# Performance work log

Hardware: AMD Instinct MI355X
Metric: run time of the kernel (lower is better)

The kernel has to match this reference:

```python
import jax, jax.numpy as jnp
import numpy as np

D = 128          # kg_emb_dim
H = 8            # mha_n_heads
N = 20000        # sub-graph nodes per modality
NNZ = 500000     # incidence entries per modality
E = 5000         # hyperedges per modality
C = 50           # context entities
NENT = 50000     # n_entity (rec vocab)


def hyperconv(x, theta, bias, nodes, edges, num_edges):
    # PyG-style HypergraphConv: out = D^-1 H B^-1 H^T (X Theta) + b
    xt = x @ theta                                             # [N, D]
    ones = jnp.ones(nodes.shape[0], xt.dtype)
    e_sum = jax.ops.segment_sum(xt[nodes], edges, num_segments=num_edges)   # [E, D]
    e_deg = jax.ops.segment_sum(ones, edges, num_segments=num_edges)        # [E]
    m = e_sum / jnp.maximum(e_deg, 1.0)[:, None]               # hyperedge means
    n_sum = jax.ops.segment_sum(m[edges], nodes, num_segments=x.shape[0])   # [N, D]
    n_deg = jax.ops.segment_sum(ones, nodes, num_segments=x.shape[0])       # [N]
    return n_sum / jnp.maximum(n_deg, 1.0)[:, None] + bias


def mha(q_x, kv_x, Wq, bq, Wk, bk, Wv, bv, Wo, bo):
    # torch.nn.MultiheadAttention math, batch of 1 (squeezed)
    dh = D // H
    q = (q_x @ Wq + bq).reshape(-1, H, dh)
    k = (kv_x @ Wk + bk).reshape(-1, H, dh)
    v = (kv_x @ Wv + bv).reshape(-1, H, dh)
    scores = jnp.einsum('qhd,khd->hqk', q, k) / jnp.sqrt(jnp.asarray(dh, q.dtype))
    attn = jax.nn.softmax(scores, axis=-1)
    out = jnp.einsum('hqk,khd->qhd', attn, v).reshape(-1, D)
    return out @ Wo + bo


def self_attn(h, a, b):
    # SelfAttentionBatch: softmax(tanh(h a) b) weighted sum over rows
    e = (jnp.tanh(h @ a) @ b)[:, 0]
    return jax.nn.softmax(e) @ h


def setup_inputs() -> dict:
    ks = jax.random.split(jax.random.key(0), 32)
    s = D ** (-0.5)
    inp = {
        'item_emb':   jax.random.normal(ks[0], (N, D), jnp.float32) * s,
        'entity_emb': jax.random.normal(ks[1], (N, D), jnp.float32) * s,
        'word_emb':   jax.random.normal(ks[2], (N, D), jnp.float32) * s,
        'context_entity': jax.random.normal(ks[3], (C, D), jnp.float32) * s,
        'theta_item':   jax.random.normal(ks[4], (D, D), jnp.float32) * s,
        'bias_item':    jax.random.normal(ks[5], (D,), jnp.float32) * 0.02,
        'theta_entity': jax.random.normal(ks[6], (D, D), jnp.float32) * s,
        'bias_entity':  jax.random.normal(ks[7], (D,), jnp.float32) * 0.02,
        'theta_word':   jax.random.normal(ks[8], (D, D), jnp.float32) * s,
        'bias_word':    jax.random.normal(ks[9], (D,), jnp.float32) * 0.02,
        'Wq': jax.random.normal(ks[10], (D, D), jnp.float32) * s,
        'bq': jax.random.normal(ks[11], (D,), jnp.float32) * 0.02,
        'Wk': jax.random.normal(ks[12], (D, D), jnp.float32) * s,
        'bk': jax.random.normal(ks[13], (D,), jnp.float32) * 0.02,
        'Wv': jax.random.normal(ks[14], (D, D), jnp.float32) * s,
        'bv': jax.random.normal(ks[15], (D,), jnp.float32) * 0.02,
        'Wo': jax.random.normal(ks[16], (D, D), jnp.float32) * s,
        'bo': jax.random.normal(ks[17], (D,), jnp.float32) * 0.02,
        'a_his': jax.random.normal(ks[18], (D, D), jnp.float32) * s,
        'b_his': jax.random.normal(ks[19], (D, 1), jnp.float32) * s,
        'a_kg':  jax.random.normal(ks[20], (D, D), jnp.float32) * s,
        'b_kg':  jax.random.normal(ks[21], (D, 1), jnp.float32) * s,
        'rec_W': jax.random.normal(ks[22], (D, NENT), jnp.float32) * s,
        'rec_b': jax.random.normal(ks[23], (NENT,), jnp.float32) * 0.02,
        'item_nodes':   jax.random.randint(ks[24], (NNZ,), 0, N, jnp.int32),
        'item_edges':   jax.random.randint(ks[25], (NNZ,), 0, E, jnp.int32),
        'entity_nodes': jax.random.randint(ks[26], (NNZ,), 0, N, jnp.int32),
        'entity_edges': jax.random.randint(ks[27], (NNZ,), 0, E, jnp.int32),
        'word_nodes':   jax.random.randint(ks[28], (NNZ,), 0, N, jnp.int32),
        'word_edges':   jax.random.randint(ks[29], (NNZ,), 0, E, jnp.int32),
    }
    return inp


def reference(item_emb, entity_emb, word_emb, context_entity,
              theta_item, bias_item, theta_entity, bias_entity, theta_word, bias_word,
              Wq, bq, Wk, bk, Wv, bv, Wo, bo,
              a_his, b_his, a_kg, b_kg, rec_W, rec_b,
              item_nodes, item_edges, entity_nodes, entity_edges, word_nodes, word_edges):
    ih = hyperconv(item_emb, theta_item, bias_item, item_nodes, item_edges, E)
    eh = hyperconv(entity_emb, theta_entity, bias_entity, entity_nodes, entity_edges, E)
    wh = hyperconv(word_emb, theta_word, bias_word, word_nodes, word_edges, E)
    related = jnp.concatenate([ih, eh, wh], axis=0)            # [3N, D]
    # MHItemAttention: context queries attend over related embeddings
    attentive = mha(context_entity, related, Wq, bq, Wk, bk, Wv, bv, Wo, bo)  # [C, D]
    u = self_attn(attentive, a_his, b_his)                     # [D]
    user = jnp.concatenate([context_entity, u[None]], axis=0)  # [C+1, D]
    user_repr = self_attn(user, a_kg, b_kg)                    # [D]
    scores = user_repr @ rec_W + rec_b                         # [NENT]
    return scores
```

## Files before the change

kernel.cpp:

```cpp
#include <hip/hip_runtime.h>
#include <hip/hip_bf16.h>

#define D_ 128
#define H_ 8
#define N_ 20000
#define NNZ_ 500000
#define E_ 5000
#define C_ 50
#define NENT_ 50000
#define NK_ (3*N_)
#define CAPE_ 192
#define CAPN_ 64
#define ENT_PB 4096
#define NBKT 157
#define BCAP 3648
#define ABLK 123
#define NCH3 118
#define KVBLK 235
#define BINA_B (3*ABLK)
#define NBB (3*NBKT)
#define EGB 3752

struct Ptr3f { const float* p[3]; };
struct Ptr3i { const int* p[3]; };
struct GemmB { const float* A[3]; const float* W[3]; unsigned short* C[3]; };

typedef short bf16x8 __attribute__((ext_vector_type(8)));
typedef float f32x4  __attribute__((ext_vector_type(4)));
typedef float f32x2  __attribute__((ext_vector_type(2)));

__device__ __forceinline__ unsigned short f2b(float f){
  unsigned u = __float_as_uint(f);
  u += 0x7FFFu + ((u>>16)&1u);
  return (unsigned short)(u>>16);
}
__device__ __forceinline__ unsigned pk2(float a, float b){
  return (unsigned)f2b(a) | ((unsigned)f2b(b) << 16);
}
__device__ __forceinline__ float blo(unsigned u){ return __uint_as_float(u<<16); }
__device__ __forceinline__ float bhi(unsigned u){ return __uint_as_float(u & 0xFFFF0000u); }

#define GBATCH(SRCB, SREG, LBASE) { \
  uint4 uu[8]; \
  _Pragma("unroll") \
  for (int kk=0;kk<8;kk++){ \
    int off = __shfl(SREG, (LBASE) + 4*kk + rgrp); \
    uu[kk] = *(const uint4*)((SRCB) + off); \
  } \
  _Pragma("unroll") \
  for (int kk=0;kk<8;kk++){ \
    a01 += (f32x2){blo(uu[kk].x), bhi(uu[kk].x)}; \
    a23 += (f32x2){blo(uu[kk].y), bhi(uu[kk].y)}; \
    a45 += (f32x2){blo(uu[kk].z), bhi(uu[kk].z)}; \
    a67 += (f32x2){blo(uu[kk].w), bhi(uu[kk].w)}; \
  } }

#define PB_PACK 7500
#define PB_Z    7628
#define PB_Q    7629
#define PB_CTX  7693
#define PB_TOT  7743
__global__ __launch_bounds__(256) void prep_binA(Ptr3f xs, unsigned short* __restrict__ xb,
    const float* __restrict__ Wk, const float* __restrict__ Wv, unsigned short* __restrict__ bfB,
    unsigned short* __restrict__ mzero,
    const float* __restrict__ ctx, const float* __restrict__ Wq, const float* __restrict__ bq,
    unsigned short* __restrict__ bfQ,
    const float* __restrict__ a2, const float* __restrict__ b2, float* __restrict__ e2,
    Ptr3i nodes, Ptr3i edges,
    unsigned* __restrict__ pe_part, unsigned* __restrict__ pn_part,
    int* __restrict__ gcnt_e, int* __restrict__ gcnt_n)
{
  const int t = threadIdx.x;
  if (blockIdx.x < BINA_B){
    __shared__ unsigned lbin[ENT_PB];
    __shared__ int cnt[256], off[256];
    __shared__ int gbase[NBKT];
    __shared__ int wsum[4];
    const int mod = blockIdx.x / ABLK;
    const int xblk = blockIdx.x - mod*ABLK;
    const int* nd = nodes.p[mod];
    const int* ed = edges.p[mod];
    const int base = xblk * ENT_PB;
    const int lane = t & 63, w = t >> 6;

    int myn[16], mye[16], pos[16];
    #pragma unroll
    for (int k=0;k<16;k++){
      int i = base + t + k*256;
      if (i < NNZ_){ myn[k]=nd[i]; mye[k]=ed[i]; }
      else { myn[k]=-1; mye[k]=-1; }
    }

    cnt[t] = 0;
    __syncthreads();
    #pragma unroll
    for (int k=0;k<16;k++)
      if (mye[k] >= 0) pos[k] = atomicAdd(&cnt[mye[k]>>5], 1);
    __syncthreads();
    {
      int v = cnt[t], s = v;
      #pragma unroll
      for (int d=1; d<64; d<<=1){ int u=__shfl_up(s,d); if (lane>=d) s+=u; }
      if (lane==63) wsum[w]=s;
      __syncthreads();
      int wb=0;
      for (int i=0;i<w;i++) wb+=wsum[i];
      off[t] = wb + s - v;
      __syncthreads();
    }
    #pragma unroll
    for (int k=0;k<16;k++)
      if (mye[k] >= 0)
        lbin[off[mye[k]>>5] + pos[k]] = ((unsigned)mye[k] << 15) | (unsigned)myn[k];
    if (t < NBKT && cnt[t] > 0) gbase[t] = atomicAdd(&gcnt_e[mod*NBKT + t], cnt[t]);
    __syncthreads();
    {
      int total = off[255];
      unsigned* dstreg = pe_part + (size_t)mod*NBKT*BCAP;
      for (int i=t; i<total; i+=256){
        unsigned pk = lbin[i];
        int b = pk >> 20;
        int gp = gbase[b] + (i - off[b]);
        if (gp < BCAP) dstreg[(size_t)b*BCAP + gp] = pk;
      }
    }
    __syncthreads();

    cnt[t] = 0;
    __syncthreads();
    #pragma unroll
    for (int k=0;k<16;k++)
      if (myn[k] >= 0) pos[k] = atomicAdd(&cnt[myn[k]>>7], 1);
    __syncthreads();
    {
      int v = cnt[t], s = v;
      #pragma unroll
      for (int d=1; d<64; d<<=1){ int u=__shfl_up(s,d); if (lane>=d) s+=u; }
      if (lane==63) wsum[w]=s;
      __syncthreads();
      int wb=0;
      for (int i=0;i<w;i++) wb+=wsum[i];
      off[t] = wb + s - v;
      __syncthreads();
    }
    #pragma unroll
    for (int k=0;k<16;k++)
      if (myn[k] >= 0)
        lbin[off[myn[k]>>7] + pos[k]] = ((unsigned)myn[k] << 13) | (unsigned)mye[k];
    if (t < NBKT && cnt[t] > 0) gbase[t] = atomicAdd(&gcnt_n[mod*NBKT + t], cnt[t]);
    __syncthreads();
    {
      int total = off[255];
      unsigned* dstreg = pn_part + (size_t)mod*NBKT*BCAP;
      for (int i=t; i<total; i+=256){
        unsigned pk = lbin[i];
        int b = pk >> 20;
        int gp = gbase[b] + (i - off[b]);
        if (gp < BCAP) dstreg[(size_t)b*BCAP + gp] = pk;
      }
    }
    return;
  }

  int bid = blockIdx.x - BINA_B;
  if (bid < PB_PACK){
    int mod = bid / 2500, blk = bid - mod*2500;
    int i4 = blk*256 + t;
    float4 v = *(const float4*)(xs.p[mod] + (size_t)i4*4);
    ushort4 o; o.x=f2b(v.x); o.y=f2b(v.y); o.z=f2b(v.z); o.w=f2b(v.w);
    *(ushort4*)(xb + (size_t)mod*N_*D_ + (size_t)i4*4) = o;
  } else if (bid < PB_Z){
    int idx = (bid - PB_PACK)*256 + t;
    int j  = idx & 7;
    int L  = (idx >> 3) & 63;
    int kb = (idx >> 9) & 3;
    int tt = idx >> 11;
    int k = kb*32 + (L>>4)*8 + j;
    int x = L & 15;
    float v = (tt < 8) ? Wk[(size_t)k*128 + tt*16 + x] : Wv[(size_t)k*128 + (tt-8)*16 + x];
    bfB[idx] = f2b(v);
  } else if (bid == PB_Z){
    if (t < 64)       ((unsigned*)(xb    + (size_t)60000*128))[t]    = 0u;
    else if (t < 128) ((unsigned*)(mzero + (size_t)15000*128))[t-64] = 0u;
  } else if (bid < PB_CTX){
    int idx = (bid - PB_Q)*256 + t;
    int j  = idx & 7;
    int L  = (idx >> 3) & 63;
    int qt = (idx >> 9) & 3;
    int h  = idx >> 11;
    int k  = ((L>>4)&3)*8 + j;
    int q  = qt*16 + (L & 15);
    float val = 0.f;
    if (k < 16 && q < C_){
      const float* cr = ctx + (size_t)q*128;
      const float* wc = Wq + h*16 + k;
      float s0=0.f,s1=0.f,s2=0.f,s3=0.f;
      for (int d=0; d<128; d+=4){
        s0 = fmaf(cr[d],   wc[(size_t) d   *128], s0);
        s1 = fmaf(cr[d+1], wc[(size_t)(d+1)*128], s1);
        s2 = fmaf(cr[d+2], wc[(size_t)(d+2)*128], s2);
        s3 = fmaf(cr[d+3], wc[(size_t)(d+3)*128], s3);
      }
      val = 0.25f * (s0+s1+s2+s3 + bq[h*16+k]);
    }
    bfQ[idx] = f2b(val);
  } else {
    __shared__ float row[128];
    __shared__ float ps[128][2];
    __shared__ float red[2];
    int q = bid - PB_CTX;
    if (t < 128) row[t] = ctx[(size_t)q*128 + t];
    __syncthreads();
    int c = t & 127, half = t >> 7;
    float s = 0.f;
    int d0 = half*64;
    for (int d=d0; d<d0+64; d+=4){
      s = fmaf(row[d],   a2[(size_t) d   *128 + c], s);
      s = fmaf(row[d+1], a2[(size_t)(d+1)*128 + c], s);
      s = fmaf(row[d+2], a2[(size_t)(d+2)*128 + c], s);
      s = fmaf(row[d+3], a2[(size_t)(d+3)*128 + c], s);
    }
    ps[c][half] = s;
    __syncthreads();
    if (t < 128){
      float v = tanhf(ps[t][0] + ps[t][1]) * b2[t];
      #pragma unroll
      for (int k=32; k>=1; k>>=1) v += __shfl_xor(v, k);
      if ((t & 63) == 0) red[t>>6] = v;
    }
    __syncthreads();
    if (t == 0) e2[q] = red[0] + red[1];
  }
}

__global__ __launch_bounds__(256) void binB_e(const unsigned* __restrict__ pe_part,
    const int* __restrict__ gcnt_e, int* __restrict__ cnt_all,
    unsigned short* __restrict__ e_slot)
{
  __shared__ unsigned short ls[32*CAPE_];
  __shared__ int lc[32];
  const int mod = blockIdx.y, b = blockIdx.x, t = threadIdx.x;
  {
    unsigned short dmy = (unsigned short)(60000 - mod*20000);
    unsigned dd = (unsigned)dmy * 0x10001u;
    unsigned* lsu32 = (unsigned*)ls;
    for (int i=t; i<32*CAPE_/2; i+=256) lsu32[i] = dd;
  }
  if (t < 32) lc[t] = 0;
  __syncthreads();
  int cnt = gcnt_e[mod*NBKT + b];
  if (cnt > BCAP) cnt = BCAP;
  const unsigned* src = pe_part + ((size_t)mod*NBKT + b)*BCAP;
  for (int i=t; i<cnt; i+=256){
    unsigned pk = src[i];
    int el = (pk >> 15) - b*32;
    int n  = pk & 0x7FFF;
    int p = atomicAdd(&lc[el], 1);
    if (p < CAPE_) ls[el*CAPE_ + p] = (unsigned short)n;
  }
  __syncthreads();
  int rows = E_ - b*32; if (rows > 32) rows = 32;
  if (t < rows) cnt_all[mod*(E_+N_) + b*32 + t] = lc[t];
  const unsigned* lsu = (const unsigned*)ls;
  unsigned* dst = (unsigned*)(e_slot + ((size_t)mod*E_ + b*32)*CAPE_);
  int tot = rows*CAPE_/2;
  for (int i=t; i<tot; i+=256) dst[i] = lsu[i];
}

__global__ __launch_bounds__(256) void egather_binbn(const unsigned short* __restrict__ xb,
    const int* __restrict__ cnt_all, const unsigned short* __restrict__ e_slot,
    float* __restrict__ m_mean,
    const unsigned* __restrict__ pn_part, const int* __restrict__ gcnt_n,
    int* __restrict__ cnt_all_w, unsigned short* __restrict__ n_slot)
{
  __shared__ unsigned short ls[128*CAPN_];
  __shared__ int lc[128];
  const int t = threadIdx.x;
  if (blockIdx.x < NBB){
    const int mod = blockIdx.x / NBKT, b = blockIdx.x - mod*NBKT;
    {
      unsigned short dmy = (unsigned short)(15000 - mod*5000);
      unsigned dd = (unsigned)dmy * 0x10001u;
      unsigned* lsu32 = (unsigned*)ls;
      for (int i=t; i<128*CAPN_/2; i+=256) lsu32[i] = dd;
    }
    if (t < 128) lc[t] = 0;
    __syncthreads();
    int cnt = gcnt_n[mod*NBKT + b];
    if (cnt > BCAP) cnt = BCAP;
    const unsigned* src = pn_part + ((size_t)mod*NBKT + b)*BCAP;
    for (int i=t; i<cnt; i+=256){
      unsigned pk = src[i];
      int nl = (pk >> 13) - b*128;
      int e  = pk & 0x1FFF;
      int p = atomicAdd(&lc[nl], 1);
      if (p < CAPN_) ls[nl*CAPN_ + p] = (unsigned short)e;
    }
    __syncthreads();
    int rows = N_ - b*128; if (rows > 128) rows = 128;
    if (t < rows) cnt_all_w[mod*(E_+N_) + E_ + b*128 + t] = lc[t];
    const unsigned* lsu = (const unsigned*)ls;
    unsigned* dst = (unsigned*)(n_slot + ((size_t)mod*N_ + b*128)*CAPN_);
    int tot = rows*CAPN_/2;
    for (int i=t; i<tot; i+=256) dst[i] = lsu[i];
    return;
  }

  const int bb = blockIdx.x - NBB;
  const int x = bb & 7, k = bb >> 3;
  int mod, r;
  if (x < 6){
    mod = x / 3;
    int li = x - mod*3;
    int c = 417 - (li == 2);
    if (k < c){
      r = k*3 + li;
    } else {
      int hg = 52*x + (x >= 3) + (k - c);
      mod = 2; r = 938 + hg;
      if (r >= E_/4) return;
    }
  } else {
    mod = 2; r = k*2 + (x - 6);
  }
  const int w = t >> 6, lane = t & 63;
  const int rgrp = lane >> 4, dl = lane & 15;
  const int e = r*4 + w;
  const char* xt8 = (const char*)(xb + (size_t)mod*N_*D_) + dl*8*2;
  int cnt = cnt_all[mod*(E_+N_) + e];
  int c2 = (cnt < CAPE_) ? cnt : CAPE_;
  int c2p = (c2 + 31) & ~31;
  const unsigned short* slot = e_slot + ((size_t)mod*E_ + e)*CAPE_;
  int sv0 = ((int)slot[lane]) << 8;
  int sv1 = ((int)slot[64 + lane]) << 8;
  int sv2 = ((int)slot[128 + lane]) << 8;
  f32x2 a01={0.f,0.f}, a23={0.f,0.f}, a45={0.f,0.f}, a67={0.f,0.f};

  if (c2p > 0)   GBATCH(xt8, sv0, 0);
  if (c2p > 32)  GBATCH(xt8, sv0, 32);
  if (c2p > 64)  GBATCH(xt8, sv1, 0);
  if (c2p > 96)  GBATCH(xt8, sv1, 32);
  if (c2p > 128) GBATCH(xt8, sv2, 0);
  if (c2p > 160) GBATCH(xt8, sv2, 32);

  float a0=a01.x, a1=a01.y, a2=a23.x, a3=a23.y, a4=a45.x, a5=a45.y, a6=a67.x, a7=a67.y;
  #pragma unroll
  for (int s=16; s<=32; s<<=1){
    a0 += __shfl_xor(a0, s); a1 += __shfl_xor(a1, s);
    a2 += __shfl_xor(a2, s); a3 += __shfl_xor(a3, s);
    a4 += __shfl_xor(a4, s); a5 += __shfl_xor(a5, s);
    a6 += __shfl_xor(a6, s); a7 += __shfl_xor(a7, s);
  }
  if (rgrp == 0){
    float inv = 1.f / fmaxf((float)cnt, 1.f);
    float* dst = m_mean + ((size_t)mod*E_ + e)*128 + dl*8;
    float4 o1; o1.x=a0*inv; o1.y=a1*inv; o1.z=a2*inv; o1.w=a3*inv;
    float4 o2; o2.x=a4*inv; o2.y=a5*inv; o2.z=a6*inv; o2.w=a7*inv;
    *(float4*)dst = o1;
    *(float4*)(dst + 4) = o2;
  }
}

__global__ __launch_bounds__(256) void gemm_b(GemmB g, int M)
{
  const float* A = g.A[blockIdx.y];
  const float* W = g.W[blockIdx.y];
  unsigned short* Cout = g.C[blockIdx.y];
  __shared__ float As[64][33];
  __shared__ float Ws[32][128];
  const int t  = threadIdx.x;
  const int br = blockIdx.x * 64;
  const int r0 = (t >> 5) * 8;
  const int c0 = (t & 31) * 4;
  const int lr = t >> 2;
  const int lk = (t & 3) * 8;
  const int wk = t >> 5;

  float acc[8][4];
  #pragma unroll
  for (int i=0;i<8;i++){ acc[i][0]=0.f; acc[i][1]=0.f; acc[i][2]=0.f; acc[i][3]=0.f; }

  for (int kb=0; kb<128; kb+=32){
    float av[8];
    const int grow = br + lr;
    if (grow < M){
      const float* p = A + (size_t)grow*128 + kb + lk;
      float4 a = ((const float4*)p)[0], b = ((const float4*)p)[1];
      av[0]=a.x;av[1]=a.y;av[2]=a.z;av[3]=a.w;av[4]=b.x;av[5]=b.y;av[6]=b.z;av[7]=b.w;
    } else {
      #pragma unroll
      for (int j=0;j<8;j++) av[j]=0.f;
    }
    float4 wv4[4];
    #pragma unroll
    for (int kk=0;kk<4;kk++) wv4[kk] = *(const float4*)&W[(size_t)(kb + wk + kk*8)*128 + c0];

    __syncthreads();
    #pragma unroll
    for (int j=0;j<8;j++) As[lr][lk+j] = av[j];
    #pragma unroll
    for (int kk=0;kk<4;kk++) *(float4*)&Ws[wk + kk*8][c0] = wv4[kk];
    __syncthreads();

    #pragma unroll
    for (int k=0;k<32;k++){
      float4 wv = *(const float4*)&Ws[k][c0];
      #pragma unroll
      for (int i=0;i<8;i++){
        float a = As[r0+i][k];
        acc[i][0] = fmaf(a, wv.x, acc[i][0]);
        acc[i][1] = fmaf(a, wv.y, acc[i][1]);
        acc[i][2] = fmaf(a, wv.z, acc[i][2]);
        acc[i][3] = fmaf(a, wv.w, acc[i][3]);
      }
    }
  }

  #pragma unroll
  for (int i=0;i<8;i++){
    int gr = br + r0 + i;
    if (gr < M){
      ushort4 o;
      o.x=f2b(acc[i][0]); o.y=f2b(acc[i][1]); o.z=f2b(acc[i][2]); o.w=f2b(acc[i][3]);
      *(ushort4*)(Cout + (size_t)gr*128 + c0) = o;
    }
  }
}

__global__ __launch_bounds__(256) void n_gather_g(const unsigned short* __restrict__ m_buf,
    const int* __restrict__ cnt_all, const unsigned short* __restrict__ n_slot,
    Ptr3f biases, unsigned short* __restrict__ relbf)
{
  const int mod = blockIdx.y;
  const int t = threadIdx.x, w = t >> 6, lane = t & 63;
  const int g = lane >> 4, dl = lane & 15;
  const int n = blockIdx.x*16 + w*4 + g;
  const char* mb = (const char*)(m_buf + (size_t)mod*E_*D_) + dl*16;
  int cnt = cnt_all[mod*(E_+N_) + E_ + n];
  int c2 = (cnt < CAPN_) ? cnt : CAPN_;
  int m = c2;
  m = max(m, __shfl_xor(m, 16));
  m = max(m, __shfl_xor(m, 32));
  int m8 = (m + 7) & ~7;
  const unsigned short* slot = n_slot + ((size_t)mod*N_ + n)*CAPN_;
  f32x2 a01={0.f,0.f}, a23={0.f,0.f}, a45={0.f,0.f}, a67={0.f,0.f};

  for (int j=0; j<m8; j+=8){
    uint4 sv = *(const uint4*)(slot + j);
    int o0 = (int)(sv.x & 0xFFFFu) << 8, o1 = (int)(sv.x >> 16) << 8;
    int o2 = (int)(sv.y & 0xFFFFu) << 8, o3 = (int)(sv.y >> 16) << 8;
    int o4 = (int)(sv.z & 0xFFFFu) << 8, o5 = (int)(sv.z >> 16) << 8;
    int o6 = (int)(sv.w & 0xFFFFu) << 8, o7 = (int)(sv.w >> 16) << 8;
    uint4 u0 = *(const uint4*)(mb + o0);
    uint4 u1 = *(const uint4*)(mb + o1);
    uint4 u2 = *(const uint4*)(mb + o2);
    uint4 u3 = *(const uint4*)(mb + o3);
    uint4 u4 = *(const uint4*)(mb + o4);
    uint4 u5 = *(const uint4*)(mb + o5);
    uint4 u6 = *(const uint4*)(mb + o6);
    uint4 u7 = *(const uint4*)(mb + o7);
    a01 += (f32x2){blo(u0.x), bhi(u0.x)}; a23 += (f32x2){blo(u0.y), bhi(u0.y)};
    a45 += (f32x2){blo(u0.z), bhi(u0.z)}; a67 += (f32x2){blo(u0.w), bhi(u0.w)};
    a01 += (f32x2){blo(u1.x), bhi(u1.x)}; a23 += (f32x2){blo(u1.y), bhi(u1.y)};
    a45 += (f32x2){blo(u1.z), bhi(u1.z)}; a67 += (f32x2){blo(u1.w), bhi(u1.w)};
    a01 += (f32x2){blo(u2.x), bhi(u2.x)}; a23 += (f32x2){blo(u2.y), bhi(u2.y)};
    a45 += (f32x2){blo(u2.z), bhi(u2.z)}; a67 += (f32x2){blo(u2.w), bhi(u2.w)};
    a01 += (f32x2){blo(u3.x), bhi(u3.x)}; a23 += (f32x2){blo(u3.y), bhi(u3.y)};
    a45 += (f32x2){blo(u3.z), bhi(u3.z)}; a67 += (f32x2){blo(u3.w), bhi(u3.w)};
    a01 += (f32x2){blo(u4.x), bhi(u4.x)}; a23 += (f32x2){blo(u4.y), bhi(u4.y)};
    a45 += (f32x2){blo(u4.z), bhi(u4.z)}; a67 += (f32x2){blo(u4.w), bhi(u4.w)};
    a01 += (f32x2){blo(u5.x), bhi(u5.x)}; a23 += (f32x2){blo(u5.y), bhi(u5.y)};
    a45 += (f32x2){blo(u5.z), bhi(u5.z)}; a67 += (f32x2){blo(u5.w), bhi(u5.w)};
    a01 += (f32x2){blo(u6.x), bhi(u6.x)}; a23 += (f32x2){blo(u6.y), bhi(u6.y)};
    a45 += (f32x2){blo(u6.z), bhi(u6.z)}; a67 += (f32x2){blo(u6.w), bhi(u6.w)};
    a01 += (f32x2){blo(u7.x), bhi(u7.x)}; a23 += (f32x2){blo(u7.y), bhi(u7.y)};
    a45 += (f32x2){blo(u7.z), bhi(u7.z)}; a67 += (f32x2){blo(u7.w), bhi(u7.w)};
  }

  float inv = 1.f / fmaxf((float)cnt, 1.f);
  const float* bs = biases.p[mod] + dl*8;
  uint4 o;
  o.x = pk2(a01.x*inv + bs[0], a01.y*inv + bs[1]);
  o.y = pk2(a23.x*inv + bs[2], a23.y*inv + bs[3]);
  o.z = pk2(a45.x*inv + bs[4], a45.y*inv + bs[5]);
  o.w = pk2(a67.x*inv + bs[6], a67.y*inv + bs[7]);
  *(uint4*)(relbf + ((size_t)mod*N_ + n)*128 + dl*8) = o;
}

__global__ __launch_bounds__(256) void gemm_kv_mfma(const unsigned short* __restrict__ relbf,
    const unsigned short* __restrict__ bfB, const float* __restrict__ bk,
    const float* __restrict__ bv, unsigned short* __restrict__ Kb,
    unsigned short* __restrict__ Vtg)
{
  __shared__ unsigned short Vs[128][72];
  const int t = threadIdx.x, w = t >> 6, L = t & 63;
  const int m = L & 15, quad = L >> 4, x = m;
  const int rowbase = blockIdx.x*256;

  for (int g = 0; g < 4; g++){
    const int j0 = rowbase + g*64 + w*16;

    bf16x8 a[4];
    {
      int row = j0 + m;
      int rowc = (row < NK_) ? row : (NK_-1);
      #pragma unroll
      for (int kb=0; kb<4; kb++)
        a[kb] = *(const bf16x8*)(relbf + (size_t)rowc*128 + kb*32 + quad*8);
    }

    f32x4 acc[16];
    #pragma unroll
    for (int tt=0; tt<16; tt++) acc[tt] = (f32x4){0.f,0.f,0.f,0.f};

    #pragma unroll
    for (int kb=0; kb<4; kb++){
      #pragma unroll
      for (int tt=0; tt<16; tt++){
        bf16x8 b = *(const bf16x8*)(bfB + (((tt*4 + kb)*64 + L) << 3));
        acc[tt] = __builtin_amdgcn_mfma_f32_16x16x32_bf16(a[kb], b, acc[tt], 0, 0, 0);
      }
    }

    #pragma unroll
    for (int tt=0; tt<8; tt++){
      float bias = bk[tt*16 + x];
      unsigned p0, p1;
      asm("v_cvt_pk_bf16_f32 %0, %1, %2" : "=v"(p0) : "v"(acc[tt][0]+bias), "v"(acc[tt][1]+bias));
      asm("v_cvt_pk_bf16_f32 %0, %1, %2" : "=v"(p1) : "v"(acc[tt][2]+bias), "v"(acc[tt][3]+bias));
      int jrb = j0 + quad*4;
      if (jrb + 3 < NK_){
        Kb[(((size_t)tt*NK_ + jrb    ) << 4) + x] = (unsigned short)p0;
        Kb[(((size_t)tt*NK_ + jrb + 1) << 4) + x] = (unsigned short)(p0 >> 16);
        Kb[(((size_t)tt*NK_ + jrb + 2) << 4) + x] = (unsigned short)p1;
        Kb[(((size_t)tt*NK_ + jrb + 3) << 4) + x] = (unsigned short)(p1 >> 16);
      } else {
        if (jrb     < NK_) Kb[(((size_t)tt*NK_ + jrb    ) << 4) + x] = (unsigned short)p0;
        if (jrb + 1 < NK_) Kb[(((size_t)tt*NK_ + jrb + 1) << 4) + x] = (unsigned short)(p0 >> 16);
        if (jrb + 2 < NK_) Kb[(((size_t)tt*NK_ + jrb + 2) << 4) + x] = (unsigned short)p1;
        if (jrb + 3 < NK_) Kb[(((size_t)tt*NK_ + jrb + 3) << 4) + x] = (unsigned short)(p1 >> 16);
      }
    }

    #pragma unroll
    for (int tt=8; tt<16; tt++){
      int h = tt - 8;
      float bias = bv[h*16 + x];
      unsigned p0, p1;
      asm("v_cvt_pk_bf16_f32 %0, %1, %2" : "=v"(p0) : "v"(acc[tt][0]+bias), "v"(acc[tt][1]+bias));
      asm("v_cvt_pk_bf16_f32 %0, %1, %2" : "=v"(p1) : "v"(acc[tt][2]+bias), "v"(acc[tt][3]+bias));
      int col = w*16 + quad*4;
      *(unsigned*)&Vs[h*16 + x][col]     = p0;
      *(unsigned*)&Vs[h*16 + x][col + 2] = p1;
    }
    __syncthreads();

    {
      int row = t >> 1, half = t & 1;
      int c0 = half*32;
      int jr0 = rowbase + g*64 + c0;
      const unsigned short* src = &Vs[row][c0];
      unsigned short* dstp = Vtg + (size_t)row*NK_ + jr0;
      if (jr0 + 31 < NK_){
        ((uint4*)dstp)[0] = ((const uint4*)src)[0];
        ((uint4*)dstp)[1] = ((const uint4*)src)[1];
        ((uint4*)dstp)[2] = ((const uint4*)src)[2];
        ((uint4*)dstp)[3] = ((const uint4*)src)[3];
      } else {
        for (int c=0; c<32; c++) if (jr0 + c < NK_) dstp[c] = src[c];
      }
    }
    __syncthreads();
  }
}

__global__ __launch_bounds__(256) void flash3(const unsigned short* __restrict__ Kb,
    const unsigned short* __restrict__ Vtg, const unsigned short* __restrict__ bfQ,
    float* __restrict__ part)
{
  __shared__ unsigned short P_lds[4][64][40];
  __shared__ float mbuf[4][64][18];
  const int c = blockIdx.x, h = blockIdx.y;
  const int t = threadIdx.x, w = t >> 6, L = t & 63;
  const int n = L & 15, quad = L >> 4;

  bf16x8 qb[4];
  #pragma unroll
  for (int qt=0; qt<4; qt++)
    qb[qt] = *(const bf16x8*)(bfQ + (((h*4 + qt)*64 + L) << 3));

  float Mc[4], Lc[4];
  f32x4 accq[4];
  #pragma unroll
  for (int qt=0; qt<4; qt++){ Mc[qt] = -INFINITY; Lc[qt] = 0.f; accq[qt] = (f32x4){0.f,0.f,0.f,0.f}; }

  const int base = c*512 + w*128;
  unsigned* Pw = (unsigned*)&P_lds[w][0][0];

  for (int tile=0; tile<4; tile++){
    const int j0 = base + tile*32;
    const bool dead = (j0 >= NK_);

    bf16x8 a0 = (bf16x8){0,0,0,0,0,0,0,0};
    bf16x8 a1 = a0;
    if (quad < 2){
      int k0 = j0 + n;      if (k0 > NK_-1) k0 = NK_-1;
      int k1 = j0 + 16 + n; if (k1 > NK_-1) k1 = NK_-1;
      a0 = *(const bf16x8*)(Kb + (((size_t)h*NK_ + k0) << 4) + quad*8);
      a1 = *(const bf16x8*)(Kb + (((size_t)h*NK_ + k1) << 4) + quad*8);
    }
    f32x4 s0[4], s1[4];
    #pragma unroll
    for (int qt=0; qt<4; qt++){
      s0[qt] = __builtin_amdgcn_mfma_f32_16x16x32_bf16(a0, qb[qt], (f32x4){0.f,0.f,0.f,0.f}, 0,0,0);
      s1[qt] = __builtin_amdgcn_mfma_f32_16x16x32_bf16(a1, qb[qt], (f32x4){0.f,0.f,0.f,0.f}, 0,0,0);
    }

    #pragma unroll
    for (int qt=0; qt<4; qt++){
      float mt = s0[qt][0];
      mt = fmaxf(mt, s0[qt][1]); mt = fmaxf(mt, s0[qt][2]); mt = fmaxf(mt, s0[qt][3]);
      mt = fmaxf(mt, s1[qt][0]); mt = fmaxf(mt, s1[qt][1]);
      mt = fmaxf(mt, s1[qt][2]); mt = fmaxf(mt, s1[qt][3]);
      mt = fmaxf(mt, __shfl_xor(mt, 16));
      mt = fmaxf(mt, __shfl_xor(mt, 32));
      float Mn = fmaxf(Mc[qt], mt);
      float corr = __expf(Mc[qt] - Mn);
      Mc[qt] = Mn;
      float p0[4], p1[4];
      #pragma unroll
      for (int r=0;r<4;r++){
        p0[r] = __expf(s0[qt][r] - Mn);
        p1[r] = __expf(s1[qt][r] - Mn);
      }
      if (dead){
        #pragma unroll
        for (int r=0;r<4;r++){ p0[r]=0.f; p1[r]=0.f; }
      }
      float lt = p0[0]+p0[1]+p0[2]+p0[3]+p1[0]+p1[1]+p1[2]+p1[3];
      lt += __shfl_xor(lt, 16);
      lt += __shfl_xor(lt, 32);
      Lc[qt] = Lc[qt]*corr + lt;
      int rb = (qt*16 + n)*20;
      Pw[rb + quad*2]     = pk2(p0[0], p0[1]);
      Pw[rb + quad*2 + 1] = pk2(p0[2], p0[3]);
      Pw[rb + 8 + quad*2]     = pk2(p1[0], p1[1]);
      Pw[rb + 8 + quad*2 + 1] = pk2(p1[2], p1[3]);
      #pragma unroll
      for (int r=0;r<4;r++){
        float cr = __shfl(corr, quad*4 + r);
        accq[qt][r] *= cr;
      }
    }
    __syncthreads();

    bf16x8 bv_;
    {
      int va = j0 + quad*8; if (va > NK_-8) va = NK_-8;
      bv_ = *(const bf16x8*)(Vtg + ((size_t)(h*16 + n))*NK_ + va);
    }
    #pragma unroll
    for (int qt=0; qt<4; qt++){
      bf16x8 pa = *(const bf16x8*)&P_lds[w][qt*16 + n][quad*8];
      accq[qt] = __builtin_amdgcn_mfma_f32_16x16x32_bf16(pa, bv_, accq[qt], 0,0,0);
    }
    __syncthreads();
  }

  #pragma unroll
  for (int qt=0; qt<4; qt++){
    #pragma unroll
    for (int r=0; r<4; r++)
      mbuf[w][qt*16 + quad*4 + r][2 + n] = accq[qt][r];
    if (quad == 0){
      mbuf[w][qt*16 + n][0] = Mc[qt];
      mbuf[w][qt*16 + n][1] = Lc[qt];
    }
  }
  __syncthreads();
  if (t < C_){
    float M = mbuf[0][t][0], Lm = mbuf[0][t][1];
    float A[16];
    #pragma unroll
    for (int i=0;i<16;i++) A[i] = mbuf[0][t][2+i];
    #pragma unroll
    for (int ww=1; ww<4; ww++){
      float pm = mbuf[ww][t][0], pl = mbuf[ww][t][1];
      if (pl > 0.f){
        float mn = fmaxf(M, pm);
        float c1 = __expf(M - mn), c2 = __expf(pm - mn);
        Lm = Lm*c1 + pl*c2;
        #pragma unroll
        for (int i=0;i<16;i++) A[i] = A[i]*c1 + mbuf[ww][t][2+i]*c2;
        M = mn;
      }
    }
    float* pp = part + ((size_t)(h*NCH3 + c)*C_ + t)*18;
    pp[0] = M; pp[1] = Lm;
    #pragma unroll
    for (int i=0;i<16;i++) pp[2+i] = A[i];
  }
}

__global__ __launch_bounds__(512) void merge_oproj_e1(const float* __restrict__ part,
    const float* __restrict__ Wo, const float* __restrict__ bo,
    const float* __restrict__ a1, const float* __restrict__ b1,
    float* __restrict__ attentive, float* __restrict__ e1)
{
  __shared__ float row[128];
  __shared__ float ps[128][4];
  __shared__ float orow[128];
  __shared__ float red[2];
  const int q = blockIdx.x, t = threadIdx.x;
  const int h = t >> 6, lane = t & 63;

  {
    float M = -1e30f, L = 0.f;
    float A[16];
    #pragma unroll
    for (int i=0;i<16;i++) A[i] = 0.f;

    #pragma unroll
    for (int cc=0; cc<2; cc++){
      int c = lane + cc*64;
      if (c < NCH3){
        const float* p = part + ((size_t)(h*NCH3 + c)*C_ + q)*18;
        float pm = p[0], pl = p[1];
        if (pl > 0.f){
          float Mn = fmaxf(M, pm);
          float w1 = __expf(M - Mn), w2 = __expf(pm - Mn);
          L = L*w1 + pl*w2;
          #pragma unroll
          for (int i=0;i<16;i++) A[i] = fmaf(A[i], w1, p[2+i]*w2);
          M = Mn;
        }
      }
    }
    #pragma unroll
    for (int d=32; d>=1; d>>=1){
      float pm = __shfl_xor(M, d);
      float pl = __shfl_xor(L, d);
      float Ao[16];
      #pragma unroll
      for (int i=0;i<16;i++) Ao[i] = __shfl_xor(A[i], d);
      float Mn = fmaxf(M, pm);
      float w1 = __expf(M - Mn), w2 = __expf(pm - Mn);
      L = L*w1 + pl*w2;
      #pragma unroll
      for (int i=0;i<16;i++) A[i] = fmaf(A[i], w1, Ao[i]*w2);
      M = Mn;
    }
    if (lane == 0){
      float invL = 1.f / L;
      #pragma unroll
      for (int i=0;i<16;i++) row[h*16 + i] = A[i]*invL;
    }
  }
  __syncthreads();

  const int c = t & 127, seg = t >> 7;
  {
    float s = 0.f;
    int d0 = seg*32;
    for (int d=d0; d<d0+32; d+=4){
      s = fmaf(row[d],   Wo[(size_t) d   *128 + c], s);
      s = fmaf(row[d+1], Wo[(size_t)(d+1)*128 + c], s);
      s = fmaf(row[d+2], Wo[(size_t)(d+2)*128 + c], s);
      s = fmaf(row[d+3], Wo[(size_t)(d+3)*128 + c], s);
    }
    ps[c][seg] = s;
  }
  __syncthreads();
  if (t < 128){
    float o = ps[t][0]+ps[t][1]+ps[t][2]+ps[t][3] + bo[t];
    attentive[(size_t)q*128 + t] = o;
    orow[t] = o;
  }
  __syncthreads();
  {
    float s = 0.f;
    int d0 = seg*32;
    for (int d=d0; d<d0+32; d+=4){
      s = fmaf(orow[d],   a1[(size_t) d   *128 + c], s);
      s = fmaf(orow[d+1], a1[(size_t)(d+1)*128 + c], s);
      s = fmaf(orow[d+2], a1[(size_t)(d+2)*128 + c], s);
      s = fmaf(orow[d+3], a1[(size_t)(d+3)*128 + c], s);
    }
    ps[c][seg] = s;
  }
  __syncthreads();
  if (t < 128){
    float v = tanhf(ps[t][0]+ps[t][1]+ps[t][2]+ps[t][3]) * b1[t];
    #pragma unroll
    for (int k=32; k>=1; k>>=1) v += __shfl_xor(v, k);
    if ((t & 63) == 0) red[t>>6] = v;
  }
  __syncthreads();
  if (t == 0) e1[q] = red[0] + red[1];
}

__global__ __launch_bounds__(256) void tail_scores(const float* __restrict__ attentive,
    const float* __restrict__ ctx, const float* __restrict__ a2, const float* __restrict__ b2,
    const float* __restrict__ e1, const float* __restrict__ e2,
    const float* __restrict__ recW, const float* __restrict__ recb, float* __restrict__ out)
{
  __shared__ float p[64];
  __shared__ float u[128];
  __shared__ float red[2];
  __shared__ float p2[64];
  __shared__ float ur[128];
  const int t = threadIdx.x;

  if (t == 0){
    float mx=-INFINITY;
    for (int i=0;i<C_;i++) mx=fmaxf(mx,e1[i]);
    float ss=0.f;
    for (int i=0;i<C_;i++){ p[i]=__expf(e1[i]-mx); ss+=p[i]; }
    float inv=1.f/ss;
    for (int i=0;i<C_;i++) p[i]*=inv;
  }
  __syncthreads();
  if (t < 128){
    float s=0.f;
    for (int r=0;r<C_;r++) s = fmaf(p[r], attentive[(size_t)r*128 + t], s);
    u[t] = s;
  }
  __syncthreads();
  if (t < 128){
    float s0=0.f,s1=0.f,s2=0.f,s3=0.f;
    for (int d=0; d<128; d+=4){
      s0 = fmaf(u[d],   a2[(size_t) d   *128 + t], s0);
      s1 = fmaf(u[d+1], a2[(size_t)(d+1)*128 + t], s1);
      s2 = fmaf(u[d+2], a2[(size_t)(d+2)*128 + t], s2);
      s3 = fmaf(u[d+3], a2[(size_t)(d+3)*128 + t], s3);
    }
    float v = tanhf(s0+s1+s2+s3) * b2[t];
    #pragma unroll
    for (int k=32; k>=1; k>>=1) v += __shfl_xor(v, k);
    if ((t & 63) == 0) red[t>>6] = v;
  }
  __syncthreads();
  if (t == 0){
    float elast = red[0] + red[1];
    float mx=elast;
    for (int i=0;i<C_;i++) mx=fmaxf(mx,e2[i]);
    float ss=0.f;
    for (int i=0;i<C_;i++){ p2[i]=__expf(e2[i]-mx); ss+=p2[i]; }
    float pl = __expf(elast-mx); ss += pl;
    float inv=1.f/ss;
    for (int i=0;i<C_;i++) p2[i]*=inv;
    p2[C_] = pl*inv;
  }
  __syncthreads();
  if (t < 128){
    float s=0.f;
    for (int r=0;r<C_;r++) s = fmaf(p2[r], ctx[(size_t)r*128 + t], s);
    s = fmaf(p2[C_], u[t], s);
    ur[t] = s;
  }
  __syncthreads();
  int j = blockIdx.x*256 + t;
  if (j < NENT_){
    float s0=0.f,s1=0.f,s2=0.f,s3=0.f;
    for (int d=0; d<128; d+=4){
      s0 = fmaf(ur[d],   recW[(size_t) d   *NENT_ + j], s0);
      s1 = fmaf(ur[d+1], recW[(size_t)(d+1)*NENT_ + j], s1);
      s2 = fmaf(ur[d+2], recW[(size_t)(d+2)*NENT_ + j], s2);
      s3 = fmaf(ur[d+3], recW[(size_t)(d+3)*NENT_ + j], s3);
    }
    out[j] = s0+s1+s2+s3 + recb[j];
  }
}

extern "C" void kernel_launch(void* const* d_in, const int* in_sizes, int n_in,
                              void* d_out, int out_size, void* d_ws, size_t ws_size,
                              hipStream_t stream)
{
  auto f32 = [&](int i){ return (const float*)d_in[i]; };
  Ptr3i nodes = {{(const int*)d_in[24], (const int*)d_in[26], (const int*)d_in[28]}};
  Ptr3i edges = {{(const int*)d_in[25], (const int*)d_in[27], (const int*)d_in[29]}};

  char* base = (char*)d_ws;
  int*   cnt_all = (int*)base;
  int*   gcnt_e  = (int*)(base + 300064);
  int*   gcnt_n  = gcnt_e + NBKT*3;
  unsigned short* n_slot = (unsigned short*)(base + 300064 + 4096);
  float* m_mean  = (float*)((char*)n_slot + 7680000);
  unsigned short* m_buf = (unsigned short*)((char*)m_mean + 7680000);
  unsigned short* relbf = (unsigned short*)((char*)m_buf + 3840256);
  unsigned short* bfB   = (unsigned short*)((char*)relbf + 15360000);
  unsigned short* bfQ   = (unsigned short*)((char*)bfB + 65536);
  float* attentive = (float*)((char*)bfQ + 32768);
  float* user_repr = (float*)((char*)attentive + 25600);
  float* e1buf     = user_repr + 128;
  float* e2buf     = e1buf + 64;
  float* fpart = (float*)relbf;
  char* U = (char*)(e2buf + 64);
  unsigned* pe_part = (unsigned*)U;
  unsigned* pn_part = pe_part + (size_t)3*NBKT*BCAP;
  unsigned short* e_slot = (unsigned short*)(pn_part + (size_t)3*NBKT*BCAP);
  unsigned short* xb     = e_slot + (size_t)3*E_*CAPE_;
  unsigned short* Kb  = (unsigned short*)U;
  unsigned short* Vtg = Kb + (size_t)H_*NK_*16;

  hipMemsetAsync(gcnt_e, 0, 4096, stream);

  Ptr3f xs = {{f32(0), f32(1), f32(2)}};
  prep_binA<<<BINA_B + PB_TOT, 256, 0, stream>>>(xs, xb, f32(12), f32(14), bfB, m_buf,
                                   f32(3), f32(10), f32(11), bfQ, f32(20), f32(21), e2buf,
                                   nodes, edges, pe_part, pn_part, gcnt_e, gcnt_n);

  binB_e<<<dim3(NBKT, 3), 256, 0, stream>>>(pe_part, gcnt_e, cnt_all, e_slot);

  egather_binbn<<<NBB + EGB, 256, 0, stream>>>(xb, cnt_all, e_slot, m_mean,
                                               pn_part, gcnt_n, cnt_all, n_slot);

  GemmB g;
  for (int mod=0; mod<3; mod++){
    g.A[mod] = m_mean + (size_t)mod*E_*D_;
    g.W[mod] = f32(4 + 2*mod);
    g.C[mod] = m_buf + (size_t)mod*E_*D_;
  }
  gemm_b<<<dim3((E_+63)/64, 3), 256, 0, stream>>>(g, E_);
  Ptr3f biases = {{f32(5), f32(7), f32(9)}};
  n_gather_g<<<dim3(N_/16, 3), 256, 0, stream>>>(m_buf, cnt_all, n_slot, biases, relbf);

  gemm_kv_mfma<<<KVBLK, 256, 0, stream>>>(relbf, bfB, f32(13), f32(15), Kb, Vtg);
  flash3<<<dim3(NCH3, H_), 256, 0, stream>>>(Kb, Vtg, bfQ, fpart);
  merge_oproj_e1<<<C_, 512, 0, stream>>>(fpart, f32(16), f32(17), f32(18), f32(19),
                                         attentive, e1buf);

  tail_scores<<<(NENT_+255)/256, 256, 0, stream>>>(attentive, f32(3), f32(20), f32(21),
                                                   e1buf, e2buf, f32(22), f32(23), (float*)d_out);
}
```

Before: 316.8 us.

## Gather hyperedge sums with one 16-lane group per edge instead of per-wave

The hyperedge-mean gather stage now assigns each hyperedge to a 16-lane group (four edges per wave, sixteen per block), looping over its incidence slots eight at a time with a shared gather macro. The old scheme used a whole wave per edge with shuffle-broadcast offsets and a cross-group shuffle reduction, plus an interleaved block-to-modality mapping. This cuts the block count and removes shuffles and reductions, but per-group loop trip counts now diverge within a wave. The node-gather kernel also drops its wave-wide max of counts, so each group loops only to its own count.

```diff
diff --git a/kernel.cpp b/kernel.cpp
--- a/kernel.cpp
+++ b/kernel.cpp
@@ -19,7 +19,7 @@
 #define KVBLK 235
 #define BINA_B (3*ABLK)
 #define NBB (3*NBKT)
-#define EGB 3752
+#define EG2 938
 
 struct Ptr3f { const float* p[3]; };
 struct Ptr3i { const int* p[3]; };
@@ -40,20 +40,37 @@
 __device__ __forceinline__ float blo(unsigned u){ return __uint_as_float(u<<16); }
 __device__ __forceinline__ float bhi(unsigned u){ return __uint_as_float(u & 0xFFFF0000u); }
 
-#define GBATCH(SRCB, SREG, LBASE) { \
-  uint4 uu[8]; \
-  _Pragma("unroll") \
-  for (int kk=0;kk<8;kk++){ \
-    int off = __shfl(SREG, (LBASE) + 4*kk + rgrp); \
-    uu[kk] = *(const uint4*)((SRCB) + off); \
-  } \
-  _Pragma("unroll") \
-  for (int kk=0;kk<8;kk++){ \
-    a01 += (f32x2){blo(uu[kk].x), bhi(uu[kk].x)}; \
-    a23 += (f32x2){blo(uu[kk].y), bhi(uu[kk].y)}; \
-    a45 += (f32x2){blo(uu[kk].z), bhi(uu[kk].z)}; \
-    a67 += (f32x2){blo(uu[kk].w), bhi(uu[kk].w)}; \
-  } }
+#define GGATHER8(MB, SLOTP, J) { \
+  uint4 sv = *(const uint4*)((SLOTP) + (J)); \
+  int o0 = (int)(sv.x & 0xFFFFu) << 8, o1 = (int)(sv.x >> 16) << 8; \
+  int o2 = (int)(sv.y & 0xFFFFu) << 8, o3 = (int)(sv.y >> 16) << 8; \
+  int o4 = (int)(sv.z & 0xFFFFu) << 8, o5 = (int)(sv.z >> 16) << 8; \
+  int o6 = (int)(sv.w & 0xFFFFu) << 8, o7 = (int)(sv.w >> 16) << 8; \
+  uint4 u0 = *(const uint4*)((MB) + o0); \
+  uint4 u1 = *(const uint4*)((MB) + o1); \
+  uint4 u2 = *(const uint4*)((MB) + o2); \
+  uint4 u3 = *(const uint4*)((MB) + o3); \
+  uint4 u4 = *(const uint4*)((MB) + o4); \
+  uint4 u5 = *(const uint4*)((MB) + o5); \
+  uint4 u6 = *(const uint4*)((MB) + o6); \
+  uint4 u7 = *(const uint4*)((MB) + o7); \
+  a01 += (f32x2){blo(u0.x), bhi(u0.x)}; a23 += (f32x2){blo(u0.y), bhi(u0.y)}; \
+  a45 += (f32x2){blo(u0.z), bhi(u0.z)}; a67 += (f32x2){blo(u0.w), bhi(u0.w)}; \
+  a01 += (f32x2){blo(u1.x), bhi(u1.x)}; a23 += (f32x2){blo(u1.y), bhi(u1.y)}; \
+  a45 += (f32x2){blo(u1.z), bhi(u1.z)}; a67 += (f32x2){blo(u1.w), bhi(u1.w)}; \
+  a01 += (f32x2){blo(u2.x), bhi(u2.x)}; a23 += (f32x2){blo(u2.y), bhi(u2.y)}; \
+  a45 += (f32x2){blo(u2.z), bhi(u2.z)}; a67 += (f32x2){blo(u2.w), bhi(u2.w)}; \
+  a01 += (f32x2){blo(u3.x), bhi(u3.x)}; a23 += (f32x2){blo(u3.y), bhi(u3.y)}; \
+  a45 += (f32x2){blo(u3.z), bhi(u3.z)}; a67 += (f32x2){blo(u3.w), bhi(u3.w)}; \
+  a01 += (f32x2){blo(u4.x), bhi(u4.x)}; a23 += (f32x2){blo(u4.y), bhi(u4.y)}; \
+  a45 += (f32x2){blo(u4.z), bhi(u4.z)}; a67 += (f32x2){blo(u4.w), bhi(u4.w)}; \
+  a01 += (f32x2){blo(u5.x), bhi(u5.x)}; a23 += (f32x2){blo(u5.y), bhi(u5.y)}; \
+  a45 += (f32x2){blo(u5.z), bhi(u5.z)}; a67 += (f32x2){blo(u5.w), bhi(u5.w)}; \
+  a01 += (f32x2){blo(u6.x), bhi(u6.x)}; a23 += (f32x2){blo(u6.y), bhi(u6.y)}; \
+  a45 += (f32x2){blo(u6.z), bhi(u6.z)}; a67 += (f32x2){blo(u6.w), bhi(u6.w)}; \
+  a01 += (f32x2){blo(u7.x), bhi(u7.x)}; a23 += (f32x2){blo(u7.y), bhi(u7.y)}; \
+  a45 += (f32x2){blo(u7.z), bhi(u7.z)}; a67 += (f32x2){blo(u7.w), bhi(u7.w)}; \
+}
 
 #define PB_PACK 7500
 #define PB_Z    7628
@@ -307,58 +324,27 @@
   }
 
   const int bb = blockIdx.x - NBB;
-  const int x = bb & 7, k = bb >> 3;
-  int mod, r;
-  if (x < 6){
-    mod = x / 3;
-    int li = x - mod*3;
-    int c = 417 - (li == 2);
-    if (k < c){
-      r = k*3 + li;
-    } else {
-      int hg = 52*x + (x >= 3) + (k - c);
-      mod = 2; r = 938 + hg;
-      if (r >= E_/4) return;
-    }
-  } else {
-    mod = 2; r = k*2 + (x - 6);
-  }
   const int w = t >> 6, lane = t & 63;
-  const int rgrp = lane >> 4, dl = lane & 15;
-  const int e = r*4 + w;
-  const char* xt8 = (const char*)(xb + (size_t)mod*N_*D_) + dl*8*2;
+  const int g = lane >> 4, dl = lane & 15;
+  int eg = bb*16 + w*4 + g;
+  if (eg >= 3*E_) return;
+  int mod = eg / E_;
+  int e = eg - mod*E_;
+  const char* mb = (const char*)(xb + (size_t)mod*N_*D_) + dl*16;
   int cnt = cnt_all[mod*(E_+N_) + e];
   int c2 = (cnt < CAPE_) ? cnt : CAPE_;
-  int c2p = (c2 + 31) & ~31;
+  int m8 = (c2 + 7) & ~7;
   const unsigned short* slot = e_slot + ((size_t)mod*E_ + e)*CAPE_;
-  int sv0 = ((int)slot[lane]) << 8;
-  int sv1 = ((int)slot[64 + lane]) << 8;
-  int sv2 = ((int)slot[128 + lane]) << 8;
   f32x2 a01={0.f,0.f}, a23={0.f,0.f}, a45={0.f,0.f}, a67={0.f,0.f};
 
-  if (c2p > 0)   GBATCH(xt8, sv0, 0);
-  if (c2p > 32)  GBATCH(xt8, sv0, 32);
-  if (c2p > 64)  GBATCH(xt8, sv1, 0);
-  if (c2p > 96)  GBATCH(xt8, sv1, 32);
-  if (c2p > 128) GBATCH(xt8, sv2, 0);
-  if (c2p > 160) GBATCH(xt8, sv2, 32);
-
-  float a0=a01.x, a1=a01.y, a2=a23.x, a3=a23.y, a4=a45.x, a5=a45.y, a6=a67.x, a7=a67.y;
-  #pragma unroll
-  for (int s=16; s<=32; s<<=1){
-    a0 += __shfl_xor(a0, s); a1 += __shfl_xor(a1, s);
-    a2 += __shfl_xor(a2, s); a3 += __shfl_xor(a3, s);
-    a4 += __shfl_xor(a4, s); a5 += __shfl_xor(a5, s);
-    a6 += __shfl_xor(a6, s); a7 += __shfl_xor(a7, s);
-  }
-  if (rgrp == 0){
-    float inv = 1.f / fmaxf((float)cnt, 1.f);
-    float* dst = m_mean + ((size_t)mod*E_ + e)*128 + dl*8;
-    float4 o1; o1.x=a0*inv; o1.y=a1*inv; o1.z=a2*inv; o1.w=a3*inv;
-    float4 o2; o2.x=a4*inv; o2.y=a5*inv; o2.z=a6*inv; o2.w=a7*inv;
-    *(float4*)dst = o1;
-    *(float4*)(dst + 4) = o2;
-  }
+  for (int j=0; j<m8; j+=8) GGATHER8(mb, slot, j)
+
+  float inv = 1.f / fmaxf((float)cnt, 1.f);
+  float* dst = m_mean + ((size_t)mod*E_ + e)*128 + dl*8;
+  float4 o1; o1.x=a01.x*inv; o1.y=a01.y*inv; o1.z=a23.x*inv; o1.w=a23.y*inv;
+  float4 o2; o2.x=a45.x*inv; o2.y=a45.y*inv; o2.z=a67.x*inv; o2.w=a67.y*inv;
+  *(float4*)dst = o1;
+  *(float4*)(dst + 4) = o2;
 }
 
 __global__ __launch_bounds__(256) void gemm_b(GemmB g, int M)
@@ -438,44 +424,11 @@
   const char* mb = (const char*)(m_buf + (size_t)mod*E_*D_) + dl*16;
   int cnt = cnt_all[mod*(E_+N_) + E_ + n];
   int c2 = (cnt < CAPN_) ? cnt : CAPN_;
-  int m = c2;
-  m = max(m, __shfl_xor(m, 16));
-  m = max(m, __shfl_xor(m, 32));
-  int m8 = (m + 7) & ~7;
+  int m8 = (c2 + 7) & ~7;
   const unsigned short* slot = n_slot + ((size_t)mod*N_ + n)*CAPN_;
   f32x2 a01={0.f,0.f}, a23={0.f,0.f}, a45={0.f,0.f}, a67={0.f,0.f};
 
-  for (int j=0; j<m8; j+=8){
-    uint4 sv = *(const uint4*)(slot + j);
-    int o0 = (int)(sv.x & 0xFFFFu) << 8, o1 = (int)(sv.x >> 16) << 8;
-    int o2 = (int)(sv.y & 0xFFFFu) << 8, o3 = (int)(sv.y >> 16) << 8;
-    int o4 = (int)(sv.z & 0xFFFFu) << 8, o5 = (int)(sv.z >> 16) << 8;
-    int o6 = (int)(sv.w & 0xFFFFu) << 8, o7 = (int)(sv.w >> 16) << 8;
-    uint4 u0 = *(const uint4*)(mb + o0);
-    uint4 u1 = *(const uint4*)(mb + o1);
-    uint4 u2 = *(const uint4*)(mb + o2);
-    uint4 u3 = *(const uint4*)(mb + o3);
-    uint4 u4 = *(const uint4*)(mb + o4);
-    uint4 u5 = *(const uint4*)(mb + o5);
-    uint4 u6 = *(const uint4*)(mb + o6);
-    uint4 u7 = *(const uint4*)(mb + o7);
-    a01 += (f32x2){blo(u0.x), bhi(u0.x)}; a23 += (f32x2){blo(u0.y), bhi(u0.y)};
-    a45 += (f32x2){blo(u0.z), bhi(u0.z)}; a67 += (f32x2){blo(u0.w), bhi(u0.w)};
-    a01 += (f32x2){blo(u1.x), bhi(u1.x)}; a23 += (f32x2){blo(u1.y), bhi(u1.y)};
-    a45 += (f32x2){blo(u1.z), bhi(u1.z)}; a67 += (f32x2){blo(u1.w), bhi(u1.w)};
-    a01 += (f32x2){blo(u2.x), bhi(u2.x)}; a23 += (f32x2){blo(u2.y), bhi(u2.y)};
-    a45 += (f32x2){blo(u2.z), bhi(u2.z)}; a67 += (f32x2){blo(u2.w), bhi(u2.w)};
-    a01 += (f32x2){blo(u3.x), bhi(u3.x)}; a23 += (f32x2){blo(u3.y), bhi(u3.y)};
-    a45 += (f32x2){blo(u3.z), bhi(u3.z)}; a67 += (f32x2){blo(u3.w), bhi(u3.w)};
-    a01 += (f32x2){blo(u4.x), bhi(u4.x)}; a23 += (f32x2){blo(u4.y), bhi(u4.y)};
-    a45 += (f32x2){blo(u4.z), bhi(u4.z)}; a67 += (f32x2){blo(u4.w), bhi(u4.w)};
-    a01 += (f32x2){blo(u5.x), bhi(u5.x)}; a23 += (f32x2){blo(u5.y), bhi(u5.y)};
-    a45 += (f32x2){blo(u5.z), bhi(u5.z)}; a67 += (f32x2){blo(u5.w), bhi(u5.w)};
-    a01 += (f32x2){blo(u6.x), bhi(u6.x)}; a23 += (f32x2){blo(u6.y), bhi(u6.y)};
-    a45 += (f32x2){blo(u6.z), bhi(u6.z)}; a67 += (f32x2){blo(u6.w), bhi(u6.w)};
-    a01 += (f32x2){blo(u7.x), bhi(u7.x)}; a23 += (f32x2){blo(u7.y), bhi(u7.y)};
-    a45 += (f32x2){blo(u7.z), bhi(u7.z)}; a67 += (f32x2){blo(u7.w), bhi(u7.w)};
-  }
+  for (int j=0; j<m8; j+=8) GGATHER8(mb, slot, j)
 
   float inv = 1.f / fmaxf((float)cnt, 1.f);
   const float* bs = biases.p[mod] + dl*8;
@@ -912,7 +865,7 @@
 
   binB_e<<<dim3(NBKT, 3), 256, 0, stream>>>(pe_part, gcnt_e, cnt_all, e_slot);
 
-  egather_binbn<<<NBB + EGB, 256, 0, stream>>>(xb, cnt_all, e_slot, m_mean,
+  egather_binbn<<<NBB + EG2, 256, 0, stream>>>(xb, cnt_all, e_slot, m_mean,
                                                pn_part, gcnt_n, cnt_all, n_slot);
 
   GemmB g;
```

New measurement: 356.6 us. +12.5%, slower.
